# Kernel tuning notes

Measured on AMD Instinct MI355X. Metric: run time of the kernel, lower is better.

## Reference

```python
import jax, jax.numpy as jnp
import numpy as np

B, S, L, F = 4, 4, 1024, 256
D, H = 256, 8
DH = D // H


def setup_inputs() -> dict:
    key = jax.random.key(0)
    ks = jax.random.split(key, 9)
    scale = 0.06  # ~1/sqrt(fan_in) init scale
    return {
        "x": jax.random.normal(ks[0], (B, S, L, F), dtype=jnp.float32),
        "Wq": jax.random.normal(ks[1], (D, F), dtype=jnp.float32) * scale,
        "bq": jnp.zeros((D,), dtype=jnp.float32),
        "Wk": jax.random.normal(ks[2], (D, F), dtype=jnp.float32) * scale,
        "bk": jnp.zeros((D,), dtype=jnp.float32),
        "Wv": jax.random.normal(ks[3], (D, F), dtype=jnp.float32) * scale,
        "bv": jnp.zeros((D,), dtype=jnp.float32),
        "Wo": jax.random.normal(ks[4], (D, D), dtype=jnp.float32) * scale,
        "bo": jnp.zeros((D,), dtype=jnp.float32),
    }


def reference(x, Wq, bq, Wk, bk, Wv, bv, Wo, bo):
    b, s, l, f = x.shape
    xr = x.reshape(b * s, l, f)  # [N, L, F] with N = batch*samples

    def split_heads(t):  # [N, L, D] -> [N, H, L, DH]
        return t.reshape(b * s, l, H, DH).transpose(0, 2, 1, 3)

    q = split_heads(xr @ Wq.T + bq)
    k = split_heads(xr @ Wk.T + bk)
    v = split_heads(xr @ Wv.T + bv)

    scores = jnp.einsum("nhqd,nhkd->nhqk", q, k) / jnp.sqrt(jnp.float32(DH))
    probs = jax.nn.softmax(scores, axis=-1)  # [N, H, L, L] — materialized as in original
    out = jnp.einsum("nhqk,nhkd->nhqd", probs, v)

    out = out.transpose(0, 2, 1, 3).reshape(b * s, l, D)
    out = out @ Wo.T + bo
    out = out.reshape(b, s, l, D)

    # softmax pooling over seq_len (dim=2)
    weight = jax.nn.softmax(out, axis=2)
    return jnp.sum(out * weight, axis=2)  # [B, S, D]
```

## Files before the change

kernel.cpp:

```cpp
#include <hip/hip_runtime.h>
#include <math.h>

#define N_SEQ 16
#define LEN   1024
#define FDIM  256
#define DDIM  256
#define NHEAD 8
#define DHD   32
#define ROWS  (N_SEQ * LEN)
#define QSCALE 0.17677669529663687f
#define QKVN  ((size_t)N_SEQ * NHEAD * LEN * DHD)

typedef __attribute__((ext_vector_type(8))) short bf16x8;
typedef __attribute__((ext_vector_type(4))) float f32x4;

__device__ __forceinline__ unsigned short f2bf(float f) {
    unsigned int u = __float_as_uint(f);
    unsigned int r = u + 0x7fffu + ((u >> 16) & 1u);
    return (unsigned short)(r >> 16);
}

__device__ __forceinline__ void load_lds16(const void* g, void* l) {
    __builtin_amdgcn_global_load_lds(
        (const __attribute__((address_space(1))) unsigned int*)g,
        (__attribute__((address_space(3))) unsigned int*)l, 16, 0, 0);
}

__global__ __launch_bounds__(256) void convert_bf16(
    const float* __restrict__ X,
    const float* __restrict__ Wq, const float* __restrict__ Wk,
    const float* __restrict__ Wv, const float* __restrict__ Wo,
    unsigned short* __restrict__ Xbf, unsigned short* __restrict__ Wbf)
{
    const size_t idx4 = ((size_t)blockIdx.x * 256 + threadIdx.x) * 4;
    const float* src;
    unsigned short* dst;
    if (idx4 < (size_t)ROWS * FDIM) {
        src = X + idx4;
        dst = Xbf + idx4;
    } else {
        const size_t wi = idx4 - (size_t)ROWS * FDIM;
        const int w = (int)(wi >> 16);
        const size_t off = wi & 65535;
        const float* Ws[4] = {Wq, Wk, Wv, Wo};
        src = Ws[w] + off;
        dst = Wbf + wi;
    }
    float4 v = *(const float4*)src;
    ushort4 u;
    u.x = f2bf(v.x); u.y = f2bf(v.y); u.z = f2bf(v.z); u.w = f2bf(v.w);
    *(ushort4*)dst = u;
}

template <int MODE>
__global__ __launch_bounds__(256) void gemm_bf16(
    const unsigned short* __restrict__ Ag, const unsigned short* __restrict__ Bg,
    const float* __restrict__ b0, const float* __restrict__ b1,
    const float* __restrict__ b2,
    unsigned short* __restrict__ OutB,
    float* __restrict__ pmO, float* __restrict__ plO, float* __restrict__ psO)
{
    __shared__ unsigned short As[16 * 512];
    __shared__ unsigned short Bs[16 * 512];

    const int m0 = blockIdx.x * 128;
    const int n0 = blockIdx.y * 128;
    const int tid  = threadIdx.x;
    const int wv   = tid >> 6;
    const int lane = tid & 63;
    const int l15  = lane & 15;
    const int quad = lane >> 4;
    const int wr = (wv & 1) * 64;
    const int wc = (wv >> 1) * 64;

    const int isB = wv >> 1;
    const unsigned short* __restrict__ Mg = isB ? Bg : Ag;
    const int mb0 = isB ? n0 : m0;
    unsigned short* Ms = isB ? Bs : As;
    const int fbase = (wv & 1) * 8;

    f32x4 acc[4][4] = {};

    for (int kt = 0; kt < 4; ++kt) {
        __syncthreads();
        #pragma unroll
        for (int f = 0; f < 8; ++f) {
            const int fi = fbase + f;
            const int i = fi >> 1, ks = fi & 1;
            load_lds16(Mg + (size_t)(mb0 + i*16 + l15) * 256 + kt*64 + ks*32 + quad*8,
                       Ms + fi * 512);
        }
        __syncthreads();
        #pragma unroll
        for (int ks = 0; ks < 2; ++ks) {
            bf16x8 af[4], bfr[4];
            #pragma unroll
            for (int i = 0; i < 4; ++i)
                af[i] = *(const bf16x8*)(&As[((((wv & 1)*4 + i)*2) + ks)*512 + lane*8]);
            #pragma unroll
            for (int j = 0; j < 4; ++j)
                bfr[j] = *(const bf16x8*)(&Bs[((((wv >> 1)*4 + j)*2) + ks)*512 + lane*8]);
            #pragma unroll
            for (int i = 0; i < 4; ++i)
                #pragma unroll
                for (int j = 0; j < 4; ++j)
                    acc[i][j] = __builtin_amdgcn_mfma_f32_16x16x32_bf16(
                        af[i], bfr[j], acc[i][j], 0, 0, 0);
        }
    }

    if (MODE == 0) {
        const int mat = n0 >> 8;
        if (mat != 2) {
            const float scale = (mat == 0) ? QSCALE : 1.0f;
            const float* __restrict__ bias = (mat == 0) ? b0 : b1;
            unsigned short* __restrict__ Out = OutB + (size_t)mat * QKVN;
            #pragma unroll
            for (int j = 0; j < 4; ++j) {
                const int c  = n0 + wc + j*16 + l15;
                const int cc = c & 255;
                const int h = cc >> 5, dh = cc & 31;
                const float bv = bias[cc];
                #pragma unroll
                for (int i = 0; i < 4; ++i)
                    #pragma unroll
                    for (int rr = 0; rr < 4; ++rr) {
                        const int r = m0 + wr + i*16 + quad*4 + rr;
                        const int n = r >> 10, l = r & 1023;
                        Out[(((size_t)(n*NHEAD + h)) * LEN + l) * DHD + dh] =
                            f2bf((acc[i][j][rr] + bv) * scale);
                    }
            }
        } else {
            unsigned short* __restrict__ Vf = OutB + 2 * QKVN;
            #pragma unroll
            for (int j = 0; j < 4; ++j) {
                const int c  = n0 + wc + j*16 + l15;
                const int cc = c & 255;
                const int h = cc >> 5, dh = cc & 31;
                const int dhb = dh >> 4, mv = dh & 15;
                const float bv = b2[cc];
                #pragma unroll
                for (int i = 0; i < 4; ++i) {
                    const int r0 = m0 + wr + i*16 + quad*4;
                    const int n = r0 >> 10, l0 = r0 & 1023;
                    const int nh = n*NHEAD + h;
                    const int kb = l0 >> 5;
                    const int qv = (l0 & 31) >> 3, jv0 = l0 & 7;
                    const size_t addr =
                        (((size_t)nh*32 + kb)*2 + dhb)*512 + (qv*16 + mv)*8 + jv0;
                    ushort4 u;
                    u.x = f2bf(acc[i][j][0] + bv);
                    u.y = f2bf(acc[i][j][1] + bv);
                    u.z = f2bf(acc[i][j][2] + bv);
                    u.w = f2bf(acc[i][j][3] + bv);
                    *(ushort4*)(Vf + addr) = u;
                }
            }
        }
    } else {
        const int n    = blockIdx.x >> 3;
        const int tile = blockIdx.x & 7;
        __shared__ float red[4][64];

        float bv[4];
        #pragma unroll
        for (int j = 0; j < 4; ++j) bv[j] = b0[n0 + wc + j*16 + l15];
        #pragma unroll
        for (int i = 0; i < 4; ++i)
            #pragma unroll
            for (int j = 0; j < 4; ++j)
                #pragma unroll
                for (int rr = 0; rr < 4; ++rr)
                    acc[i][j][rr] += bv[j];

        float M[4];
        #pragma unroll
        for (int j = 0; j < 4; ++j) {
            float m = -1e30f;
            #pragma unroll
            for (int i = 0; i < 4; ++i)
                #pragma unroll
                for (int rr = 0; rr < 4; ++rr) m = fmaxf(m, acc[i][j][rr]);
            m = fmaxf(m, __shfl_xor(m, 16));
            m = fmaxf(m, __shfl_xor(m, 32));
            M[j] = m;
        }
        if (quad == 0) {
            #pragma unroll
            for (int j = 0; j < 4; ++j) red[wv][j*16 + l15] = M[j];
        }
        __syncthreads();
        #pragma unroll
        for (int j = 0; j < 4; ++j)
            M[j] = fmaxf(red[wv][j*16 + l15], red[wv^1][j*16 + l15]);
        __syncthreads();

        float LE[4], SE[4];
        #pragma unroll
        for (int j = 0; j < 4; ++j) {
            float le = 0.f, se = 0.f;
            #pragma unroll
            for (int i = 0; i < 4; ++i)
                #pragma unroll
                for (int rr = 0; rr < 4; ++rr) {
                    const float z = acc[i][j][rr];
                    const float e = __expf(z - M[j]);
                    le += e; se += z * e;
                }
            le += __shfl_xor(le, 16); le += __shfl_xor(le, 32);
            se += __shfl_xor(se, 16); se += __shfl_xor(se, 32);
            LE[j] = le; SE[j] = se;
        }
        if (quad == 0) {
            #pragma unroll
            for (int j = 0; j < 4; ++j) red[wv][j*16 + l15] = LE[j];
        }
        __syncthreads();
        float LEp[4];
        #pragma unroll
        for (int j = 0; j < 4; ++j) LEp[j] = red[wv^1][j*16 + l15];
        __syncthreads();
        if (quad == 0) {
            #pragma unroll
            for (int j = 0; j < 4; ++j) red[wv][j*16 + l15] = SE[j];
        }
        __syncthreads();
        float SEp[4];
        #pragma unroll
        for (int j = 0; j < 4; ++j) SEp[j] = red[wv^1][j*16 + l15];

        if ((wv & 1) == 0 && quad == 0) {
            #pragma unroll
            for (int j = 0; j < 4; ++j) {
                const int c = n0 + wc + j*16 + l15;
                const size_t o = ((size_t)n*8 + tile)*256 + c;
                pmO[o] = M[j];
                plO[o] = LE[j] + LEp[j];
                psO[o] = SE[j] + SEp[j];
            }
        }
    }
}

#define LDPk 72
__global__ __launch_bounds__(256) void attn_mfma(
    const unsigned short* __restrict__ Qg_, const unsigned short* __restrict__ Kg_,
    const unsigned short* __restrict__ Vf_, unsigned short* __restrict__ Aout)
{
    __shared__ unsigned short Pb[4][16 * LDPk];

    const int nh = blockIdx.y;
    const int n  = nh >> 3, h = nh & 7;
    const int q0 = blockIdx.x * 256;
    const int tid  = threadIdx.x;
    const int wv   = tid >> 6;
    const int lane = tid & 63;
    const int l15  = lane & 15;
    const int quad = lane >> 4;

    const unsigned short* __restrict__ Qg = Qg_ + (size_t)nh * LEN * DHD;
    const unsigned short* __restrict__ Kg = Kg_ + (size_t)nh * LEN * DHD;
    const unsigned short* __restrict__ Vf = Vf_ + (size_t)nh * 32768;

    bf16x8 qf[4];
    #pragma unroll
    for (int g = 0; g < 4; ++g)
        qf[g] = *(const bf16x8*)(Qg + (size_t)(q0 + wv*64 + g*16 + l15) * DHD + quad*8);

    f32x4 oA[4] = {{0.f,0.f,0.f,0.f},{0.f,0.f,0.f,0.f},{0.f,0.f,0.f,0.f},{0.f,0.f,0.f,0.f}};
    f32x4 oB[4] = {{0.f,0.f,0.f,0.f},{0.f,0.f,0.f,0.f},{0.f,0.f,0.f,0.f},{0.f,0.f,0.f,0.f}};
    float l_acc[4] = {0.f, 0.f, 0.f, 0.f};

    const unsigned short* __restrict__ kbase = Kg + (size_t)l15 * DHD + quad*8;
    const unsigned short* __restrict__ vbase = Vf + lane*8;

    bf16x8 kf[4], vv[4];
    #pragma unroll
    for (int s = 0; s < 4; ++s) kf[s] = *(const bf16x8*)(kbase + (size_t)(s*16) * DHD);
    #pragma unroll
    for (int j = 0; j < 4; ++j) vv[j] = *(const bf16x8*)(vbase + j*512);

    unsigned short* __restrict__ Pw = &Pb[wv][0];

    for (int t = 0; t < 16; ++t) {
        bf16x8 kn[4], vn[4];
        if (t < 15) {
            #pragma unroll
            for (int s = 0; s < 4; ++s)
                kn[s] = *(const bf16x8*)(kbase + (size_t)((t+1)*64 + s*16) * DHD);
            #pragma unroll
            for (int j = 0; j < 4; ++j)
                vn[j] = *(const bf16x8*)(vbase + ((t+1)*4 + j)*512);
        }
        #pragma unroll
        for (int g = 0; g < 4; ++g) {
            f32x4 st[4];
            #pragma unroll
            for (int s = 0; s < 4; ++s) {
                f32x4 z = {0.f, 0.f, 0.f, 0.f};
                st[s] = __builtin_amdgcn_mfma_f32_16x16x32_bf16(kf[s], qf[g], z, 0, 0, 0);
            }
            float lg = 0.f;
            #pragma unroll
            for (int s = 0; s < 4; ++s) {
                const unsigned int a0 = __float_as_uint(__expf(st[s][0])) & 0xffff0000u;
                const unsigned int a1 = __float_as_uint(__expf(st[s][1])) & 0xffff0000u;
                const unsigned int a2 = __float_as_uint(__expf(st[s][2])) & 0xffff0000u;
                const unsigned int a3 = __float_as_uint(__expf(st[s][3])) & 0xffff0000u;
                lg += (__uint_as_float(a0) + __uint_as_float(a1))
                    + (__uint_as_float(a2) + __uint_as_float(a3));
                uint2 pk;
                pk.x = (a0 >> 16) | a1;
                pk.y = (a2 >> 16) | a3;
                *(uint2*)(&Pw[l15*LDPk + s*16 + quad*4]) = pk;
            }
            l_acc[g] += lg;
            #pragma unroll
            for (int kk = 0; kk < 2; ++kk) {
                bf16x8 pf = *(const bf16x8*)(&Pw[l15*LDPk + kk*32 + quad*8]);
                oA[g] = __builtin_amdgcn_mfma_f32_16x16x32_bf16(vv[kk*2+0], pf, oA[g], 0, 0, 0);
                oB[g] = __builtin_amdgcn_mfma_f32_16x16x32_bf16(vv[kk*2+1], pf, oB[g], 0, 0, 0);
            }
        }
        if (t < 15) {
            #pragma unroll
            for (int s = 0; s < 4; ++s) kf[s] = kn[s];
            #pragma unroll
            for (int j = 0; j < 4; ++j) vv[j] = vn[j];
        }
    }

    float linv[4];
    #pragma unroll
    for (int g = 0; g < 4; ++g) {
        float tsum = l_acc[g];
        tsum += __shfl_xor(tsum, 16);
        tsum += __shfl_xor(tsum, 32);
        linv[g] = 1.f / tsum;
    }

    float* __restrict__ Tw = (float*)&Pb[wv][0];
    const int qr = lane >> 2, c8 = (lane & 3) * 8;
    #pragma unroll
    for (int g = 0; g < 4; ++g) {
        #pragma unroll
        for (int r = 0; r < 4; ++r) {
            Tw[l15*36 + quad*4 + r]      = oA[g][r] * linv[g];
            Tw[l15*36 + 16 + quad*4 + r] = oB[g][r] * linv[g];
        }
        float4 r0 = *(const float4*)(&Tw[qr*36 + c8]);
        float4 r1 = *(const float4*)(&Tw[qr*36 + c8 + 4]);
        unsigned short* dst =
            Aout + ((size_t)(n*LEN + q0 + wv*64 + g*16 + qr)) * DDIM + h*DHD + c8;
        ushort4 u0, u1;
        u0.x = f2bf(r0.x); u0.y = f2bf(r0.y); u0.z = f2bf(r0.z); u0.w = f2bf(r0.w);
        u1.x = f2bf(r1.x); u1.y = f2bf(r1.y); u1.z = f2bf(r1.z); u1.w = f2bf(r1.w);
        *(ushort4*)(dst)     = u0;
        *(ushort4*)(dst + 4) = u1;
    }
}

__global__ __launch_bounds__(256) void pool_merge(
    const float* __restrict__ pm, const float* __restrict__ pl,
    const float* __restrict__ ps, float* __restrict__ out)
{
    const int n = blockIdx.x;
    const int d = threadIdx.x;
    float M = -1e30f;
    #pragma unroll
    for (int t = 0; t < 8; ++t) M = fmaxf(M, pm[((size_t)n*8 + t)*256 + d]);
    float L = 0.f, S = 0.f;
    #pragma unroll
    for (int t = 0; t < 8; ++t) {
        const size_t idx = ((size_t)n*8 + t)*256 + d;
        const float w = __expf(pm[idx] - M);
        L += pl[idx] * w;
        S += ps[idx] * w;
    }
    out[n*256 + d] = S / L;
}

extern "C" void kernel_launch(void* const* d_in, const int* in_sizes, int n_in,
                              void* d_out, int out_size, void* d_ws, size_t ws_size,
                              hipStream_t stream)
{
    const float* x  = (const float*)d_in[0];
    const float* Wq = (const float*)d_in[1];
    const float* bq = (const float*)d_in[2];
    const float* Wk = (const float*)d_in[3];
    const float* bk = (const float*)d_in[4];
    const float* Wv = (const float*)d_in[5];
    const float* bv = (const float*)d_in[6];
    const float* Wo = (const float*)d_in[7];
    const float* bo = (const float*)d_in[8];
    float* out = (float*)d_out;

    char* base = (char*)d_ws;
    unsigned short* Xbf  = (unsigned short*)(base);
    unsigned short* Qb   = (unsigned short*)(base +  8388608);
    unsigned short* Vfrag= (unsigned short*)(base + 25165824);
    unsigned short* attnb= (unsigned short*)(base + 41943040);
    unsigned short* Wbf  = (unsigned short*)(base + 50331648);
    float* pm = (float*)(base + 50855936);
    float* pl = (float*)(base + 50987008);
    float* ps = (float*)(base + 51118080);
    const size_t need_bytes = 51249152;
    if (ws_size < need_bytes) return;

    convert_bf16<<<4352, 256, 0, stream>>>(x, Wq, Wk, Wv, Wo, Xbf, Wbf);
    gemm_bf16<0><<<dim3(ROWS/128, 6), 256, 0, stream>>>(
        Xbf, Wbf, bq, bk, bv, Qb, nullptr, nullptr, nullptr);
    attn_mfma<<<dim3(LEN/256, N_SEQ*NHEAD), 256, 0, stream>>>(
        Qb, Qb + QKVN, Vfrag, attnb);
    gemm_bf16<1><<<dim3(ROWS/128, 2), 256, 0, stream>>>(
        attnb, Wbf + (size_t)768*256, bo, nullptr, nullptr, nullptr, pm, pl, ps);
    pool_merge<<<16, 256, 0, stream>>>(pm, pl, ps, out);
}
```

Baseline: 140.8 us.

## Double-buffer P tiles in attention, use exp2 with folded log2e, transpose QK GEMM

The attention inner loop now writes P into two alternating LDS buffers, so the PV MFMAs for query group g-1 are issued after group g's score/exp work. This software-pipelines the LDS round trip against compute. The exponent becomes a native exp2 with log2(e) folded into the Q scale, and bf16 packing uses a single perm instead of masks and shifts. The Q/K projection GEMM swaps operands so each lane holds four consecutive head dims, allowing vectorized ushort4 stores, at the cost of more LDS and register pressure.

```diff
diff --git a/kernel.cpp b/kernel.cpp
--- a/kernel.cpp
+++ b/kernel.cpp
@@ -9,6 +9,7 @@
 #define DHD   32
 #define ROWS  (N_SEQ * LEN)
 #define QSCALE 0.17677669529663687f
+#define LOG2E  1.4426950408889634f
 #define QKVN  ((size_t)N_SEQ * NHEAD * LEN * DHD)
 
 typedef __attribute__((ext_vector_type(8))) short bf16x8;
@@ -18,6 +19,16 @@
     unsigned int u = __float_as_uint(f);
     unsigned int r = u + 0x7fffu + ((u >> 16) & 1u);
     return (unsigned short)(r >> 16);
+}
+
+#if __has_builtin(__builtin_amdgcn_exp2f)
+#define EXP2F(x) __builtin_amdgcn_exp2f(x)
+#else
+#define EXP2F(x) __expf((x) * 0.6931471805599453f)
+#endif
+
+__device__ __forceinline__ unsigned int pack_bf16_trunc(float p0, float p1) {
+    return __builtin_amdgcn_perm(__float_as_uint(p1), __float_as_uint(p0), 0x07060302u);
 }
 
 __device__ __forceinline__ void load_lds16(const void* g, void* l) {
@@ -63,8 +74,6 @@
     __shared__ unsigned short As[16 * 512];
     __shared__ unsigned short Bs[16 * 512];
 
-    const int m0 = blockIdx.x * 128;
-    const int n0 = blockIdx.y * 128;
     const int tid  = threadIdx.x;
     const int wv   = tid >> 6;
     const int lane = tid & 63;
@@ -73,9 +82,27 @@
     const int wr = (wv & 1) * 64;
     const int wc = (wv >> 1) * 64;
 
+    int mat = 0, cb = 0, abase, bbase;
+    const unsigned short* __restrict__ Astage;
+    const unsigned short* __restrict__ Bstage;
+    if (MODE == 0) {
+        mat = blockIdx.y >> 1;
+        cb  = (blockIdx.y & 1) * 128;
+        if (mat < 2) {
+            Astage = Bg + (size_t)mat * 65536; abase = cb;
+            Bstage = Ag;                       bbase = blockIdx.x * 128;
+        } else {
+            Astage = Ag;                       abase = blockIdx.x * 128;
+            Bstage = Bg + (size_t)2 * 65536;   bbase = cb;
+        }
+    } else {
+        Astage = Ag; abase = blockIdx.x * 128;
+        Bstage = Bg; bbase = blockIdx.y * 128;
+    }
+
     const int isB = wv >> 1;
-    const unsigned short* __restrict__ Mg = isB ? Bg : Ag;
-    const int mb0 = isB ? n0 : m0;
+    const unsigned short* __restrict__ Mg = isB ? Bstage : Astage;
+    const int mb0 = isB ? bbase : abase;
     unsigned short* Ms = isB ? Bs : As;
     const int fbase = (wv & 1) * 8;
 
@@ -110,39 +137,38 @@
     }
 
     if (MODE == 0) {
-        const int mat = n0 >> 8;
-        if (mat != 2) {
-            const float scale = (mat == 0) ? QSCALE : 1.0f;
+        if (mat < 2) {
+            const float scale = (mat == 0) ? QSCALE * LOG2E : 1.0f;
             const float* __restrict__ bias = (mat == 0) ? b0 : b1;
             unsigned short* __restrict__ Out = OutB + (size_t)mat * QKVN;
             #pragma unroll
-            for (int j = 0; j < 4; ++j) {
-                const int c  = n0 + wc + j*16 + l15;
-                const int cc = c & 255;
-                const int h = cc >> 5, dh = cc & 31;
-                const float bv = bias[cc];
-                #pragma unroll
-                for (int i = 0; i < 4; ++i)
-                    #pragma unroll
-                    for (int rr = 0; rr < 4; ++rr) {
-                        const int r = m0 + wr + i*16 + quad*4 + rr;
-                        const int n = r >> 10, l = r & 1023;
-                        Out[(((size_t)(n*NHEAD + h)) * LEN + l) * DHD + dh] =
-                            f2bf((acc[i][j][rr] + bv) * scale);
-                    }
+            for (int i = 0; i < 4; ++i) {
+                const int c0 = cb + wr + i*16 + quad*4;
+                const int h = c0 >> 5, dh = c0 & 31;
+                const float4 bv4 = *(const float4*)(bias + c0);
+                #pragma unroll
+                for (int j = 0; j < 4; ++j) {
+                    const int r = bbase + wc + j*16 + l15;
+                    const int n = r >> 10, l = r & 1023;
+                    ushort4 u;
+                    u.x = f2bf((acc[i][j][0] + bv4.x) * scale);
+                    u.y = f2bf((acc[i][j][1] + bv4.y) * scale);
+                    u.z = f2bf((acc[i][j][2] + bv4.z) * scale);
+                    u.w = f2bf((acc[i][j][3] + bv4.w) * scale);
+                    *(ushort4*)(Out + ((size_t)(n*NHEAD + h) * LEN + l) * DHD + dh) = u;
+                }
             }
         } else {
             unsigned short* __restrict__ Vf = OutB + 2 * QKVN;
             #pragma unroll
             for (int j = 0; j < 4; ++j) {
-                const int c  = n0 + wc + j*16 + l15;
-                const int cc = c & 255;
+                const int cc = cb + wc + j*16 + l15;
                 const int h = cc >> 5, dh = cc & 31;
                 const int dhb = dh >> 4, mv = dh & 15;
                 const float bv = b2[cc];
                 #pragma unroll
                 for (int i = 0; i < 4; ++i) {
-                    const int r0 = m0 + wr + i*16 + quad*4;
+                    const int r0 = abase + wr + i*16 + quad*4;
                     const int n = r0 >> 10, l0 = r0 & 1023;
                     const int nh = n*NHEAD + h;
                     const int kb = l0 >> 5;
@@ -165,7 +191,7 @@
 
         float bv[4];
         #pragma unroll
-        for (int j = 0; j < 4; ++j) bv[j] = b0[n0 + wc + j*16 + l15];
+        for (int j = 0; j < 4; ++j) bv[j] = b0[bbase + wc + j*16 + l15];
         #pragma unroll
         for (int i = 0; i < 4; ++i)
             #pragma unroll
@@ -233,7 +259,7 @@
         if ((wv & 1) == 0 && quad == 0) {
             #pragma unroll
             for (int j = 0; j < 4; ++j) {
-                const int c = n0 + wc + j*16 + l15;
+                const int c = bbase + wc + j*16 + l15;
                 const size_t o = ((size_t)n*8 + tile)*256 + c;
                 pmO[o] = M[j];
                 plO[o] = LE[j] + LEp[j];
@@ -248,7 +274,7 @@
     const unsigned short* __restrict__ Qg_, const unsigned short* __restrict__ Kg_,
     const unsigned short* __restrict__ Vf_, unsigned short* __restrict__ Aout)
 {
-    __shared__ unsigned short Pb[4][16 * LDPk];
+    __shared__ unsigned short Pb[4][2][16 * LDPk];
 
     const int nh = blockIdx.y;
     const int n  = nh >> 3, h = nh & 7;
@@ -281,7 +307,8 @@
     #pragma unroll
     for (int j = 0; j < 4; ++j) vv[j] = *(const bf16x8*)(vbase + j*512);
 
-    unsigned short* __restrict__ Pw = &Pb[wv][0];
+    unsigned short* __restrict__ Pw0 = &Pb[wv][0][0];
+    unsigned short* __restrict__ Pw1 = &Pb[wv][1][0];
 
     for (int t = 0; t < 16; ++t) {
         bf16x8 kn[4], vn[4];
@@ -295,33 +322,49 @@
         }
         #pragma unroll
         for (int g = 0; g < 4; ++g) {
+            unsigned short* __restrict__ Pcur  = (g & 1) ? Pw1 : Pw0;
+            unsigned short* __restrict__ Pprev = (g & 1) ? Pw0 : Pw1;
             f32x4 st[4];
             #pragma unroll
             for (int s = 0; s < 4; ++s) {
                 f32x4 z = {0.f, 0.f, 0.f, 0.f};
                 st[s] = __builtin_amdgcn_mfma_f32_16x16x32_bf16(kf[s], qf[g], z, 0, 0, 0);
             }
+            uint2 pk[4];
             float lg = 0.f;
             #pragma unroll
             for (int s = 0; s < 4; ++s) {
-                const unsigned int a0 = __float_as_uint(__expf(st[s][0])) & 0xffff0000u;
-                const unsigned int a1 = __float_as_uint(__expf(st[s][1])) & 0xffff0000u;
-                const unsigned int a2 = __float_as_uint(__expf(st[s][2])) & 0xffff0000u;
-                const unsigned int a3 = __float_as_uint(__expf(st[s][3])) & 0xffff0000u;
-                lg += (__uint_as_float(a0) + __uint_as_float(a1))
-                    + (__uint_as_float(a2) + __uint_as_float(a3));
-                uint2 pk;
-                pk.x = (a0 >> 16) | a1;
-                pk.y = (a2 >> 16) | a3;
-                *(uint2*)(&Pw[l15*LDPk + s*16 + quad*4]) = pk;
+                const float p0 = EXP2F(st[s][0]);
+                const float p1 = EXP2F(st[s][1]);
+                const float p2 = EXP2F(st[s][2]);
+                const float p3 = EXP2F(st[s][3]);
+                lg += (p0 + p1) + (p2 + p3);
+                pk[s].x = pack_bf16_trunc(p0, p1);
+                pk[s].y = pack_bf16_trunc(p2, p3);
             }
             l_acc[g] += lg;
-            #pragma unroll
-            for (int kk = 0; kk < 2; ++kk) {
-                bf16x8 pf = *(const bf16x8*)(&Pw[l15*LDPk + kk*32 + quad*8]);
-                oA[g] = __builtin_amdgcn_mfma_f32_16x16x32_bf16(vv[kk*2+0], pf, oA[g], 0, 0, 0);
-                oB[g] = __builtin_amdgcn_mfma_f32_16x16x32_bf16(vv[kk*2+1], pf, oB[g], 0, 0, 0);
-            }
+            bf16x8 pf0, pf1;
+            if (g > 0) {
+                pf0 = *(const bf16x8*)(&Pprev[l15*LDPk + 0*32 + quad*8]);
+                pf1 = *(const bf16x8*)(&Pprev[l15*LDPk + 1*32 + quad*8]);
+            }
+            #pragma unroll
+            for (int s = 0; s < 4; ++s)
+                *(uint2*)(&Pcur[l15*LDPk + s*16 + quad*4]) = pk[s];
+            if (g > 0) {
+                oA[g-1] = __builtin_amdgcn_mfma_f32_16x16x32_bf16(vv[0], pf0, oA[g-1], 0, 0, 0);
+                oB[g-1] = __builtin_amdgcn_mfma_f32_16x16x32_bf16(vv[1], pf0, oB[g-1], 0, 0, 0);
+                oA[g-1] = __builtin_amdgcn_mfma_f32_16x16x32_bf16(vv[2], pf1, oA[g-1], 0, 0, 0);
+                oB[g-1] = __builtin_amdgcn_mfma_f32_16x16x32_bf16(vv[3], pf1, oB[g-1], 0, 0, 0);
+            }
+        }
+        {
+            bf16x8 pf0 = *(const bf16x8*)(&Pw1[l15*LDPk + 0*32 + quad*8]);
+            bf16x8 pf1 = *(const bf16x8*)(&Pw1[l15*LDPk + 1*32 + quad*8]);
+            oA[3] = __builtin_amdgcn_mfma_f32_16x16x32_bf16(vv[0], pf0, oA[3], 0, 0, 0);
+            oB[3] = __builtin_amdgcn_mfma_f32_16x16x32_bf16(vv[1], pf0, oB[3], 0, 0, 0);
+            oA[3] = __builtin_amdgcn_mfma_f32_16x16x32_bf16(vv[2], pf1, oA[3], 0, 0, 0);
+            oB[3] = __builtin_amdgcn_mfma_f32_16x16x32_bf16(vv[3], pf1, oB[3], 0, 0, 0);
         }
         if (t < 15) {
             #pragma unroll
@@ -340,7 +383,7 @@
         linv[g] = 1.f / tsum;
     }
 
-    float* __restrict__ Tw = (float*)&Pb[wv][0];
+    float* __restrict__ Tw = (float*)&Pb[wv][0][0];
     const int qr = lane >> 2, c8 = (lane & 3) * 8;
     #pragma unroll
     for (int g = 0; g < 4; ++g) {
```

After: 139.1 us. No clear change (-1.3%).
